# Kernel optimization log

Hardware: AMD Instinct MI355X
Metric: run time of the kernel (lower is better)

The kernel has to match this reference:

```python
import jax, jax.numpy as jnp
import numpy as np

OLD_CL = 16
RATIO = 1.0
IGNORE_INDEX = 255


def setup_inputs() -> dict:
    key = jax.random.key(0)
    k1, k2 = jax.random.split(key)
    N, C, H, W = 8, 21, 512, 512
    inputs = jax.random.normal(k1, (N, C, H, W), dtype=jnp.float32)
    targets = jax.random.randint(k2, (N, H, W), 0, C).astype(jnp.int32)
    return {"inputs": inputs, "targets": targets}


def _forward(inputs, targets):
    N, C, H, W = inputs.shape
    # unbiased log-prob remap: old classes collapsed into channel 0
    den = jax.nn.logsumexp(inputs, axis=1)                       # [N,H,W]
    out0 = jax.nn.logsumexp(inputs[:, :OLD_CL], axis=1) - den    # [N,H,W]
    outputs = jnp.zeros_like(inputs)                             # channels 1..OLD_CL-1 stay 0
    outputs = outputs.at[:, 0].set(out0)
    outputs = outputs.at[:, OLD_CL:].set(inputs[:, OLD_CL:] - den[:, None])

    labels = jnp.where(targets < OLD_CL, 0, targets)             # [N,H,W]

    # per-sample class histogram (device-side replacement for the per-sample
    # cpu torch.histc loop). histc(bins=C, min=0, max=C-1) on integer-valued
    # labels counts occurrences per class, dropping values outside [0, C-1].
    lab_flat = labels.reshape(N, -1)
    in_range = lab_flat < C
    seg = jnp.where(in_range, lab_flat, 0) + jnp.arange(N, dtype=lab_flat.dtype)[:, None] * C
    hist = jax.ops.segment_sum(
        in_range.astype(jnp.float32).reshape(-1), seg.reshape(-1), num_segments=N * C
    ).reshape(N, C)

    cls = jnp.arange(C)
    idx_old = (cls < OLD_CL) & (cls != 0)                        # [C], old classes except 0
    idx0 = hist == 0                                             # computed on raw hist
    hist = hist.at[:, 0].set(hist[:, :OLD_CL].sum(axis=1))
    hist = jnp.where(idx_old[None, :], 0.0, hist)
    hist = jnp.where(idx0 & ~idx_old[None, :], 1.0, hist)
    weight = jnp.power(hist.sum(axis=1, keepdims=True) / hist, RATIO)
    weight = jnp.where(idx_old[None, :], 0.0, weight)            # kills the infs from /0
    weight = jax.lax.stop_gradient(weight)                       # torch .detach()

    outputs = outputs * weight[:, :, None, None]

    # nll_loss with ignore_index, mean reduction over valid pixels
    valid = labels != IGNORE_INDEX
    safe = jnp.where(valid, labels, 0)
    picked = jnp.take_along_axis(outputs, safe[:, None], axis=1)[:, 0]  # [N,H,W]
    vmask = valid.astype(outputs.dtype)
    return -(picked * vmask).sum() / vmask.sum()


def reference(inputs, targets):
    return _forward(inputs, targets)
```

## Files before the change

### kernel.cpp

```cpp
#include <hip/hip_runtime.h>

#define NS 8
#define NC 21
#define HW (512*512)
#define OLD 16
#define IGNORE_IDX 255

#define HIST_OFF 0
#define WGT_OFF  1024
#define SUM_OFF  2048
#define CNT_OFF  2056
#define WS_BYTES 4096

__device__ __forceinline__ float get4(const float4& v, int j) {
    switch (j) { case 0: return v.x; case 1: return v.y; case 2: return v.z; default: return v.w; }
}

__global__ void __launch_bounds__(256) hist_kernel(const int* __restrict__ tgt,
                                                   int* __restrict__ hist) {
    int n   = blockIdx.x >> 6;
    int blk = blockIdx.x & 63;
    const int4* t4 = reinterpret_cast<const int4*>(tgt + (size_t)n * HW);
    int c0 = 0, c16 = 0, c17 = 0, c18 = 0, c19 = 0, c20 = 0;
#pragma unroll
    for (int it = 0; it < 4; ++it) {
        int idx = blk * 1024 + it * 256 + threadIdx.x;
        int4 t = t4[idx];
#define COUNT_LAB(T) { int lab = (T) < OLD ? 0 : (T);                      \
        c0  += (lab == 0);  c16 += (lab == 16); c17 += (lab == 17);        \
        c18 += (lab == 18); c19 += (lab == 19); c20 += (lab == 20); }
        COUNT_LAB(t.x) COUNT_LAB(t.y) COUNT_LAB(t.z) COUNT_LAB(t.w)
#undef COUNT_LAB
    }
#pragma unroll
    for (int off = 32; off > 0; off >>= 1) {
        c0  += __shfl_down(c0,  off, 64);
        c16 += __shfl_down(c16, off, 64);
        c17 += __shfl_down(c17, off, 64);
        c18 += __shfl_down(c18, off, 64);
        c19 += __shfl_down(c19, off, 64);
        c20 += __shfl_down(c20, off, 64);
    }
    if ((threadIdx.x & 63) == 0) {
        int* h = hist + n * NC;
        atomicAdd(&h[0],  c0);
        atomicAdd(&h[16], c16);
        atomicAdd(&h[17], c17);
        atomicAdd(&h[18], c18);
        atomicAdd(&h[19], c19);
        atomicAdd(&h[20], c20);
    }
}

__device__ __forceinline__ float adj_hist(const int* h, int k) {
    if (k >= 1 && k < OLD) return 0.0f;
    int raw = h[k];
    if (k == 0) {
        int s = 0;
        for (int j = 0; j < OLD; ++j) s += h[j];
        float v = (float)s;
        if (raw == 0) v = 1.0f;
        return v;
    }
    return raw == 0 ? 1.0f : (float)raw;
}

__global__ void weight_kernel(const int* __restrict__ hist, float* __restrict__ wgt) {
    int i = threadIdx.x;
    if (i >= NS * NC) return;
    int n = i / NC, c = i % NC;
    const int* h = hist + n * NC;
    float total = 0.0f;
    for (int k = 0; k < NC; ++k) total += adj_hist(h, k);
    float w;
    if (c >= 1 && c < OLD) w = 0.0f;
    else                   w = total / adj_hist(h, c);
    wgt[i] = w;
}

__global__ void __launch_bounds__(256) loss_kernel(const float* __restrict__ in,
                                                   const int* __restrict__ tgt,
                                                   const float* __restrict__ wgt,
                                                   double* __restrict__ sum_acc,
                                                   int* __restrict__ cnt_acc) {
    const int perN = HW / 4;
    int gid = blockIdx.x * 256 + threadIdx.x;
    int n   = gid / perN;
    int p   = (gid - n * perN) * 4;

    __shared__ float sw[NC];
    if (threadIdx.x < NC) sw[threadIdx.x] = wgt[n * NC + threadIdx.x];
    __syncthreads();

    const float* base = in + (size_t)n * (NC * HW) + p;
    int4 t = *reinterpret_cast<const int4*>(tgt + (size_t)n * HW + p);

    float4 v[NC];
#pragma unroll
    for (int c = 0; c < NC; ++c)
        v[c] = *reinterpret_cast<const float4*>(base + (size_t)c * HW);

    int labs[4] = {t.x, t.y, t.z, t.w};
    float partial = 0.0f;
    int cnt = 0;
#pragma unroll
    for (int j = 0; j < 4; ++j) {
        int lab = labs[j];
        lab = lab < OLD ? 0 : lab;
        float m16 = -3.4e38f;
#pragma unroll
        for (int c = 0; c < OLD; ++c) m16 = fmaxf(m16, get4(v[c], j));
        float s16 = 0.0f;
#pragma unroll
        for (int c = 0; c < OLD; ++c) s16 += __expf(get4(v[c], j) - m16);
        float m = m16;
#pragma unroll
        for (int c = OLD; c < NC; ++c) m = fmaxf(m, get4(v[c], j));
        float s  = s16 * __expf(m16 - m);
        float xl = 0.0f;
#pragma unroll
        for (int c = OLD; c < NC; ++c) {
            float x = get4(v[c], j);
            s += __expf(x - m);
            xl = (lab == c) ? x : xl;
        }
        float den   = m + __logf(s);
        float lse16 = m16 + __logf(s16);
        float val   = (lab == 0 ? lse16 : xl) - den;
        int  widx   = (lab < NC) ? lab : 0;
        bool valid  = (lab != IGNORE_IDX);
        if (valid) { partial += sw[widx] * val; cnt++; }
    }

#pragma unroll
    for (int off = 32; off > 0; off >>= 1) {
        partial += __shfl_down(partial, off, 64);
        cnt     += __shfl_down(cnt, off, 64);
    }
    __shared__ float sp[4];
    __shared__ int   sc[4];
    int wave = threadIdx.x >> 6;
    if ((threadIdx.x & 63) == 0) { sp[wave] = partial; sc[wave] = cnt; }
    __syncthreads();
    if (threadIdx.x == 0) {
        float ps = sp[0] + sp[1] + sp[2] + sp[3];
        int   pc = sc[0] + sc[1] + sc[2] + sc[3];
        atomicAdd(sum_acc, (double)ps);
        atomicAdd(cnt_acc, pc);
    }
}

__global__ void finalize_kernel(const double* __restrict__ sum_acc,
                                const int* __restrict__ cnt_acc,
                                float* __restrict__ out) {
    if (threadIdx.x == 0) {
        int c = *cnt_acc;
        out[0] = (c > 0) ? (float)(-(*sum_acc) / (double)c) : 0.0f;
    }
}

extern "C" void kernel_launch(void* const* d_in, const int* in_sizes, int n_in,
                              void* d_out, int out_size, void* d_ws, size_t ws_size,
                              hipStream_t stream) {
    const float* inputs  = (const float*)d_in[0];
    const int*   targets = (const int*)d_in[1];
    float*       out     = (float*)d_out;

    char* ws = (char*)d_ws;
    int*    hist    = (int*)(ws + HIST_OFF);
    float*  wgt     = (float*)(ws + WGT_OFF);
    double* sum_acc = (double*)(ws + SUM_OFF);
    int*    cnt_acc = (int*)(ws + CNT_OFF);

    hipMemsetAsync(d_ws, 0, WS_BYTES, stream);

    hist_kernel<<<NS * 64, 256, 0, stream>>>(targets, hist);
    weight_kernel<<<1, 192, 0, stream>>>(hist, wgt);
    loss_kernel<<<(NS * HW / 4) / 256, 256, 0, stream>>>(inputs, targets, wgt, sum_acc, cnt_acc);
    finalize_kernel<<<1, 64, 0, stream>>>(sum_acc, cnt_acc, out);
}
```

Measured before the change: 281.9 us.

## Replace atomics and memset with per-block partials and last-block reduction

Removes the workspace memset and the separate finalize kernel. Histogram blocks now write per-block partial counts that the weight kernel sums, and the weight kernel also resets a ticket counter. The loss kernel writes per-block partial sums, and the last block to arrive (found via an atomic ticket) does the final reduction and writes the output. This cuts two launches and the contended double atomics, but adds a threadfence/ticket protocol and a serial final reduction in one block.

```diff
diff --git a/kernel.cpp b/kernel.cpp
--- a/kernel.cpp
+++ b/kernel.cpp
@@ -5,84 +5,92 @@
 #define HW (512*512)
 #define OLD 16
 #define IGNORE_IDX 255
-
-#define HIST_OFF 0
-#define WGT_OFF  1024
-#define SUM_OFF  2048
-#define CNT_OFF  2056
-#define WS_BYTES 4096
+#define HBLK 64
+#define LGRID (NS * (HW/4) / 256)
+
+#define HPART_OFF  0
+#define WGT_OFF    16384
+#define PSUM_OFF   17408
+#define PCNT_OFF   25600
+#define TICKET_OFF 33792
 
 __device__ __forceinline__ float get4(const float4& v, int j) {
     switch (j) { case 0: return v.x; case 1: return v.y; case 2: return v.z; default: return v.w; }
 }
 
 __global__ void __launch_bounds__(256) hist_kernel(const int* __restrict__ tgt,
-                                                   int* __restrict__ hist) {
+                                                   int* __restrict__ hpart) {
     int n   = blockIdx.x >> 6;
     int blk = blockIdx.x & 63;
     const int4* t4 = reinterpret_cast<const int4*>(tgt + (size_t)n * HW);
-    int c0 = 0, c16 = 0, c17 = 0, c18 = 0, c19 = 0, c20 = 0;
+    int c[6] = {0, 0, 0, 0, 0, 0};
 #pragma unroll
     for (int it = 0; it < 4; ++it) {
         int idx = blk * 1024 + it * 256 + threadIdx.x;
         int4 t = t4[idx];
-#define COUNT_LAB(T) { int lab = (T) < OLD ? 0 : (T);                      \
-        c0  += (lab == 0);  c16 += (lab == 16); c17 += (lab == 17);        \
-        c18 += (lab == 18); c19 += (lab == 19); c20 += (lab == 20); }
+#define COUNT_LAB(T) { int lab = (T) < OLD ? 0 : (T);                       \
+        c[0] += (lab == 0);  c[1] += (lab == 16); c[2] += (lab == 17);      \
+        c[3] += (lab == 18); c[4] += (lab == 19); c[5] += (lab == 20); }
         COUNT_LAB(t.x) COUNT_LAB(t.y) COUNT_LAB(t.z) COUNT_LAB(t.w)
 #undef COUNT_LAB
     }
 #pragma unroll
-    for (int off = 32; off > 0; off >>= 1) {
-        c0  += __shfl_down(c0,  off, 64);
-        c16 += __shfl_down(c16, off, 64);
-        c17 += __shfl_down(c17, off, 64);
-        c18 += __shfl_down(c18, off, 64);
-        c19 += __shfl_down(c19, off, 64);
-        c20 += __shfl_down(c20, off, 64);
-    }
-    if ((threadIdx.x & 63) == 0) {
-        int* h = hist + n * NC;
-        atomicAdd(&h[0],  c0);
-        atomicAdd(&h[16], c16);
-        atomicAdd(&h[17], c17);
-        atomicAdd(&h[18], c18);
-        atomicAdd(&h[19], c19);
-        atomicAdd(&h[20], c20);
-    }
-}
-
-__device__ __forceinline__ float adj_hist(const int* h, int k) {
-    if (k >= 1 && k < OLD) return 0.0f;
-    int raw = h[k];
-    if (k == 0) {
+    for (int off = 32; off > 0; off >>= 1)
+#pragma unroll
+        for (int k = 0; k < 6; ++k) c[k] += __shfl_down(c[k], off, 64);
+
+    __shared__ int sh[4][6];
+    int wave = threadIdx.x >> 6;
+    if ((threadIdx.x & 63) == 0)
+#pragma unroll
+        for (int k = 0; k < 6; ++k) sh[wave][k] = c[k];
+    __syncthreads();
+    if (threadIdx.x == 0) {
+        int* out = hpart + blockIdx.x * 8;
+#pragma unroll
+        for (int k = 0; k < 6; ++k)
+            out[k] = sh[0][k] + sh[1][k] + sh[2][k] + sh[3][k];
+    }
+}
+
+__global__ void weight_kernel(const int* __restrict__ hpart,
+                              float* __restrict__ wgt,
+                              unsigned int* __restrict__ ticket) {
+    __shared__ int shist[NS][6];
+    int t = threadIdx.x;
+    if (t < NS * 6) {
+        int n = t / 6, k = t % 6;
         int s = 0;
-        for (int j = 0; j < OLD; ++j) s += h[j];
-        float v = (float)s;
-        if (raw == 0) v = 1.0f;
-        return v;
-    }
-    return raw == 0 ? 1.0f : (float)raw;
-}
-
-__global__ void weight_kernel(const int* __restrict__ hist, float* __restrict__ wgt) {
-    int i = threadIdx.x;
-    if (i >= NS * NC) return;
-    int n = i / NC, c = i % NC;
-    const int* h = hist + n * NC;
-    float total = 0.0f;
-    for (int k = 0; k < NC; ++k) total += adj_hist(h, k);
-    float w;
-    if (c >= 1 && c < OLD) w = 0.0f;
-    else                   w = total / adj_hist(h, c);
-    wgt[i] = w;
+        for (int b = 0; b < HBLK; ++b) s += hpart[(n * HBLK + b) * 8 + k];
+        shist[n][k] = s;
+    }
+    if (t == 0) *ticket = 0;
+    __syncthreads();
+    if (t < NS * NC) {
+        int n = t / NC, c = t % NC;
+        float h[6];
+        float total = 0.0f;
+#pragma unroll
+        for (int k = 0; k < 6; ++k) {
+            int raw = shist[n][k];
+            h[k] = (raw == 0) ? 1.0f : (float)raw;
+            total += h[k];
+        }
+        float w;
+        if (c >= 1 && c < OLD)      w = 0.0f;
+        else if (c == 0)            w = total / h[0];
+        else                        w = total / h[c - OLD + 1];
+        wgt[t] = w;
+    }
 }
 
 __global__ void __launch_bounds__(256) loss_kernel(const float* __restrict__ in,
                                                    const int* __restrict__ tgt,
                                                    const float* __restrict__ wgt,
-                                                   double* __restrict__ sum_acc,
-                                                   int* __restrict__ cnt_acc) {
+                                                   float* __restrict__ psum,
+                                                   int* __restrict__ pcnt,
+                                                   unsigned int* __restrict__ ticket,
+                                                   float* __restrict__ out) {
     const int perN = HW / 4;
     int gid = blockIdx.x * 256 + threadIdx.x;
     int n   = gid / perN;
@@ -139,23 +147,43 @@
     }
     __shared__ float sp[4];
     __shared__ int   sc[4];
+    __shared__ bool  amLast;
     int wave = threadIdx.x >> 6;
     if ((threadIdx.x & 63) == 0) { sp[wave] = partial; sc[wave] = cnt; }
     __syncthreads();
     if (threadIdx.x == 0) {
-        float ps = sp[0] + sp[1] + sp[2] + sp[3];
-        int   pc = sc[0] + sc[1] + sc[2] + sc[3];
-        atomicAdd(sum_acc, (double)ps);
-        atomicAdd(cnt_acc, pc);
-    }
-}
-
-__global__ void finalize_kernel(const double* __restrict__ sum_acc,
-                                const int* __restrict__ cnt_acc,
-                                float* __restrict__ out) {
-    if (threadIdx.x == 0) {
-        int c = *cnt_acc;
-        out[0] = (c > 0) ? (float)(-(*sum_acc) / (double)c) : 0.0f;
+        psum[blockIdx.x] = sp[0] + sp[1] + sp[2] + sp[3];
+        pcnt[blockIdx.x] = sc[0] + sc[1] + sc[2] + sc[3];
+        __threadfence();
+        unsigned int tk = atomicAdd(ticket, 1u);
+        amLast = (tk == (unsigned int)(LGRID - 1));
+    }
+    __syncthreads();
+
+    if (amLast) {
+        __threadfence();
+        const volatile float* vs = (const volatile float*)psum;
+        const volatile int*   vc = (const volatile int*)pcnt;
+        double dsum = 0.0;
+        long long dcnt = 0;
+        for (int i = threadIdx.x; i < LGRID; i += 256) {
+            dsum += (double)vs[i];
+            dcnt += vc[i];
+        }
+#pragma unroll
+        for (int off = 32; off > 0; off >>= 1) {
+            dsum += __shfl_down(dsum, off, 64);
+            dcnt += __shfl_down(dcnt, off, 64);
+        }
+        __shared__ double fs[4];
+        __shared__ long long fc[4];
+        if ((threadIdx.x & 63) == 0) { fs[wave] = dsum; fc[wave] = dcnt; }
+        __syncthreads();
+        if (threadIdx.x == 0) {
+            double S = fs[0] + fs[1] + fs[2] + fs[3];
+            long long Cn = fc[0] + fc[1] + fc[2] + fc[3];
+            out[0] = (Cn > 0) ? (float)(-S / (double)Cn) : 0.0f;
+        }
     }
 }
 
@@ -167,15 +195,13 @@
     float*       out     = (float*)d_out;
 
     char* ws = (char*)d_ws;
-    int*    hist    = (int*)(ws + HIST_OFF);
-    float*  wgt     = (float*)(ws + WGT_OFF);
-    double* sum_acc = (double*)(ws + SUM_OFF);
-    int*    cnt_acc = (int*)(ws + CNT_OFF);
-
-    hipMemsetAsync(d_ws, 0, WS_BYTES, stream);
-
-    hist_kernel<<<NS * 64, 256, 0, stream>>>(targets, hist);
-    weight_kernel<<<1, 192, 0, stream>>>(hist, wgt);
-    loss_kernel<<<(NS * HW / 4) / 256, 256, 0, stream>>>(inputs, targets, wgt, sum_acc, cnt_acc);
-    finalize_kernel<<<1, 64, 0, stream>>>(sum_acc, cnt_acc, out);
-}
+    int*          hpart  = (int*)(ws + HPART_OFF);
+    float*        wgt    = (float*)(ws + WGT_OFF);
+    float*        psum   = (float*)(ws + PSUM_OFF);
+    int*          pcnt   = (int*)(ws + PCNT_OFF);
+    unsigned int* ticket = (unsigned int*)(ws + TICKET_OFF);
+
+    hist_kernel<<<NS * HBLK, 256, 0, stream>>>(targets, hpart);
+    weight_kernel<<<1, 256, 0, stream>>>(hpart, wgt, ticket);
+    loss_kernel<<<LGRID, 256, 0, stream>>>(inputs, targets, wgt, psum, pcnt, ticket, out);
+}
```

Measured after the change: 355.1 us. +26.0%, slower.
